# Optimization experiments

Hardware: AMD Instinct MI355X
Metric: run time of the kernel (lower is better)

## Reference

```python
import jax, jax.numpy as jnp
import numpy as np

FP4_MAX = 6.0
FP8_MAX = 448.0  # float8_e4m3fn max
BLOCK = 16
# representable |values| of fp4 e2m1 and decision midpoints (ties round up)
FP4_LEVELS = jnp.array([0.0, 0.5, 1.0, 1.5, 2.0, 3.0, 4.0, 6.0], dtype=jnp.float32)
FP4_MIDS = jnp.array([0.25, 0.75, 1.25, 1.75, 2.5, 3.5, 5.0], dtype=jnp.float32)


def _fp4_round(x):
    # round to nearest fp4 e2m1 value (magnitudes clamp at 6)
    a = jnp.abs(x)
    idx = jnp.searchsorted(FP4_MIDS, a, side='right')
    return jnp.sign(x) * FP4_LEVELS[idx]


def nvfp4_quant(x, global_scale):
    # x: [M, K] float32 -> (q_fp4 values [M, K], block scales [M, K//16] fp8-representable)
    M, K = x.shape
    xb = x.reshape(M, K // BLOCK, BLOCK)
    block_amax = jnp.max(jnp.abs(xb), axis=-1)  # [M, K//16]
    scale = jnp.clip(block_amax * (global_scale / FP4_MAX), 0.0, FP8_MAX)
    scale = scale.astype(jnp.float8_e4m3fn).astype(jnp.float32)
    safe = jnp.where(scale == 0.0, 1.0, scale)
    q = _fp4_round(xb * (global_scale / safe)[..., None])
    return q.reshape(M, K), scale


def setup_inputs() -> dict:
    key = jax.random.key(0)
    k_in, k_w, k_b = jax.random.split(key, 3)
    M, K, N = 256, 5120, 13824
    x = jax.random.normal(k_in, (M, K), dtype=jnp.float32)
    # build pre-quantized NVFP4 weight buffers (as the module's load_quantized_weights would)
    w = jax.random.normal(k_w, (N, K), dtype=jnp.float32) * 0.02
    w_gs = (FP8_MAX * FP4_MAX) / jnp.max(jnp.abs(w))  # scalar float32
    w_fp4, w_scale = nvfp4_quant(w, w_gs)
    bias = jax.random.normal(k_b, (N,), dtype=jnp.float32) * 0.01
    return {
        'input': x,
        'weight_fp4': w_fp4,            # [N, K] fp4 values held in f32
        'weight_scale': w_scale,        # [N, K//16] fp8_e4m3-representable f32
        'weight_global_scale': w_gs,    # scalar f32
        'bias': bias,                   # [N]
    }


def reference(input, weight_fp4, weight_scale, weight_global_scale, bias):
    # activations cast to bf16 (as in the torch module), math in f32
    x = input.astype(jnp.bfloat16).astype(jnp.float32)
    M, K = x.shape
    N = weight_fp4.shape[0]
    # per-tensor global scale for activations
    a_gs = (FP8_MAX * FP4_MAX) / jnp.max(jnp.abs(x))
    alpha = 1.0 / (a_gs * weight_global_scale)
    # on-the-fly fp4 quantization of activations
    a_fp4, a_scale = nvfp4_quant(x, a_gs)
    # block-scaled dequant-matmul: out = (a_fp4*s_a) @ (w_fp4*s_w)^T * alpha + bias
    a_u = (a_fp4.reshape(M, K // BLOCK, BLOCK) * a_scale[..., None]).reshape(M, K)
    w_u = (weight_fp4.reshape(N, K // BLOCK, BLOCK) * weight_scale[..., None]).reshape(N, K)
    out = jnp.einsum('mk,nk->mn', a_u, w_u) * alpha + bias[None, :]
    return out
```

## Files before the change

kernel.cpp:

```cpp
#include <hip/hip_runtime.h>

typedef __attribute__((ext_vector_type(8))) __bf16 bf16x8;
typedef __attribute__((ext_vector_type(4))) __bf16 bf16x4;
typedef __attribute__((ext_vector_type(4))) float floatx4;

#define M_TOT 256
#define K_TOT 5120
#define N_TOT 13824
#define NBLK  320
#define BN    64
#define BK    32
#define KSPLIT 4
#define KCH   1280
#define NSTEP 40

#define GLOAD_LDS16(g, l)                                                     \
  __builtin_amdgcn_global_load_lds(                                           \
      (const __attribute__((address_space(1))) void*)(g),                     \
      (__attribute__((address_space(3))) void*)(l), 16, 0, 0)

static __device__ __forceinline__ float bf16r(float v) { return (float)(__bf16)v; }

static __device__ __forceinline__ float fp4round(float v) {
  float a = fabsf(v), q;
  if      (a < 0.25f) q = 0.0f;
  else if (a < 0.75f) q = 0.5f;
  else if (a < 1.25f) q = 1.0f;
  else if (a < 1.75f) q = 1.5f;
  else if (a < 2.5f)  q = 2.0f;
  else if (a < 3.5f)  q = 3.0f;
  else if (a < 5.0f)  q = 4.0f;
  else                q = 6.0f;
  return copysignf(q, v);
}

static __device__ __forceinline__ float cvt_e4m3(float f) {
  if (f < 0.015625f) return rintf(f * 512.0f) * 0.001953125f;
  int e = (int)(__float_as_uint(f) >> 23) - 127;
  float q = __uint_as_float((unsigned)(e - 3 + 127) << 23);
  return rintf(f / q) * q;
}

__global__ void k_zero(float4* __restrict__ out4) {
  int idx = blockIdx.x * blockDim.x + threadIdx.x;
#pragma unroll
  for (int i = 0; i < 4; ++i) out4[idx + i * 221184] = (float4){0.f, 0.f, 0.f, 0.f};
}

__global__ void k_amax(const float* __restrict__ x, unsigned* __restrict__ amax_bits) {
  int i = blockIdx.x * blockDim.x + threadIdx.x;
  float4 v = ((const float4*)x)[i];
  float m = fmaxf(fmaxf(fabsf(bf16r(v.x)), fabsf(bf16r(v.y))),
                  fmaxf(fabsf(bf16r(v.z)), fabsf(bf16r(v.w))));
#pragma unroll
  for (int off = 32; off; off >>= 1) m = fmaxf(m, __shfl_xor(m, off));
  if ((threadIdx.x & 63) == 0) atomicMax(amax_bits, __float_as_uint(m));
}

__global__ void k_aquant(const float* __restrict__ x,
                         const unsigned* __restrict__ amax_bits,
                         __bf16* __restrict__ au) {
  int idx = blockIdx.x * blockDim.x + threadIdx.x;
  int m = idx / NBLK;
  int b = idx - m * NBLK;
  float amax = __uint_as_float(*amax_bits);
  float gs  = 2688.0f / amax;
  float gs6 = gs / 6.0f;
  const float4* xp = (const float4*)(x + m * K_TOT + b * 16);
  float4 v0 = xp[0], v1 = xp[1], v2 = xp[2], v3 = xp[3];
  float xv[16];
  xv[0]=bf16r(v0.x); xv[1]=bf16r(v0.y); xv[2]=bf16r(v0.z); xv[3]=bf16r(v0.w);
  xv[4]=bf16r(v1.x); xv[5]=bf16r(v1.y); xv[6]=bf16r(v1.z); xv[7]=bf16r(v1.w);
  xv[8]=bf16r(v2.x); xv[9]=bf16r(v2.y); xv[10]=bf16r(v2.z); xv[11]=bf16r(v2.w);
  xv[12]=bf16r(v3.x); xv[13]=bf16r(v3.y); xv[14]=bf16r(v3.z); xv[15]=bf16r(v3.w);
  float am = 0.f;
#pragma unroll
  for (int j = 0; j < 16; ++j) am = fmaxf(am, fabsf(xv[j]));
  float s = cvt_e4m3(fminf(am * gs6, 448.0f));
  float g = gs / ((s == 0.f) ? 1.f : s);
  bf16x8 p0, p1;
#pragma unroll
  for (int j = 0; j < 8; ++j) p0[j] = (__bf16)(fp4round(xv[j] * g) * s);
#pragma unroll
  for (int j = 0; j < 8; ++j) p1[j] = (__bf16)(fp4round(xv[8 + j] * g) * s);
  bf16x8* dst = (bf16x8*)(au + (size_t)idx * 16);
  dst[0] = p0; dst[1] = p1;
}

__global__ __launch_bounds__(512, 4) void k_gemm(
    const __bf16* __restrict__ au,
    const float*  __restrict__ w,
    const float*  __restrict__ wsc,
    const unsigned* __restrict__ amax_bits,
    const float*  __restrict__ wgs,
    const float*  __restrict__ bias,
    float* __restrict__ out)
{
  __shared__ __bf16 Ab[2][M_TOT * BK];
  __shared__ __bf16 Bb[2][BN * BK];

  const int tid  = threadIdx.x;
  const int lane = tid & 63;
  const int wv   = tid >> 6;
  const int wm   = wv >> 1;
  const int wn   = wv & 1;

  const int s     = blockIdx.x & (KSPLIT - 1);
  const int n0    = (blockIdx.x >> 2) * BN;
  const int kbase = s * KCH;

  const int arow  = wv * 32 + (lane >> 2);
  const int acolp = 8 * ((lane & 3) ^ ((lane >> 2) & 3));

  const int brow = tid >> 3;
  const int bcg  = tid & 7;
  const float* wp  = w   + (size_t)(n0 + brow) * K_TOT + kbase + bcg * 4;
  const float* wsp = wsc + (size_t)(n0 + brow) * NBLK + s * (KCH / 16);
  const int bsci = bcg >> 2;
  const int bdst = brow * 64 + (((bcg >> 1) ^ (brow & 3)) << 4) + (bcg & 1) * 8;

  const int hi  = lane >> 4;
  const int r15 = lane & 15;
  const int sw3 = r15 & 3;

  floatx4 acc[4][2];
#pragma unroll
  for (int fm = 0; fm < 4; ++fm)
#pragma unroll
    for (int fn = 0; fn < 2; ++fn) acc[fm][fn] = (floatx4){0.f, 0.f, 0.f, 0.f};

  float4 bv; float bs;

  auto issueA = [&](int t, int buf) {
    const __bf16* src = au + (size_t)arow * K_TOT + kbase + t * BK + acolp;
    char* dst = (char*)(&Ab[buf][0]) + wv * 2048;
#pragma unroll
    for (int i = 0; i < 2; ++i)
      GLOAD_LDS16(src + (size_t)i * 16 * K_TOT, dst + i * 1024);
  };
  auto loadB = [&](int t) {
    bv = *(const float4*)(wp + t * BK);
    bs = wsp[t * 2 + bsci];
  };
  auto writeB = [&](int buf) {
    bf16x4 pk;
    pk[0] = (__bf16)(bv.x * bs); pk[1] = (__bf16)(bv.y * bs);
    pk[2] = (__bf16)(bv.z * bs); pk[3] = (__bf16)(bv.w * bs);
    *(bf16x4*)((char*)(&Bb[buf][0]) + bdst) = pk;
  };
  auto compute = [&](int buf) {
    char* pA = (char*)(&Ab[buf][0]);
    char* pB = (char*)(&Bb[buf][0]);
    bf16x8 af[4], bfr[2];
#pragma unroll
    for (int fm = 0; fm < 4; ++fm) {
      const int row = wm * 64 + fm * 16 + r15;
      af[fm] = *(const bf16x8*)(pA + row * 64 + ((hi ^ sw3) << 4));
    }
#pragma unroll
    for (int fn = 0; fn < 2; ++fn) {
      const int row = wn * 32 + fn * 16 + r15;
      bfr[fn] = *(const bf16x8*)(pB + row * 64 + ((hi ^ sw3) << 4));
    }
#pragma unroll
    for (int fm = 0; fm < 4; ++fm)
#pragma unroll
      for (int fn = 0; fn < 2; ++fn)
        acc[fm][fn] = __builtin_amdgcn_mfma_f32_16x16x32_bf16(af[fm], bfr[fn], acc[fm][fn], 0, 0, 0);
  };

  int buf = 0;
  issueA(0, 0);
  loadB(0);
  writeB(0);
  __syncthreads();
#pragma unroll 1
  for (int t = 0; t < NSTEP; ++t) {
    if (t + 1 < NSTEP) { issueA(t + 1, buf ^ 1); loadB(t + 1); }
    compute(buf);
    if (t + 1 < NSTEP) writeB(buf ^ 1);
    __syncthreads();
    buf ^= 1;
  }

  float amax = __uint_as_float(*amax_bits);
  float a_gs = 2688.0f / amax;
  float alpha = 1.0f / (a_gs * wgs[0]);
#pragma unroll
  for (int fm = 0; fm < 4; ++fm) {
#pragma unroll
    for (int fn = 0; fn < 2; ++fn) {
      int mrow = wm * 64 + fm * 16 + hi * 4;
      int ncol = n0 + wn * 32 + fn * 16 + r15;
      float bb = (s == 0) ? bias[ncol] : 0.0f;
#pragma unroll
      for (int j = 0; j < 4; ++j)
        atomicAdd(&out[(size_t)(mrow + j) * N_TOT + ncol],
                  acc[fm][fn][j] * alpha + bb);
    }
  }
}

extern "C" void kernel_launch(void* const* d_in, const int* in_sizes, int n_in,
                              void* d_out, int out_size, void* d_ws, size_t ws_size,
                              hipStream_t stream) {
  const float* x    = (const float*)d_in[0];
  const float* wq   = (const float*)d_in[1];
  const float* wsc  = (const float*)d_in[2];
  const float* wgs  = (const float*)d_in[3];
  const float* bias = (const float*)d_in[4];
  float* out = (float*)d_out;

  unsigned* amax = (unsigned*)d_ws;
  __bf16* au = (__bf16*)((char*)d_ws + 256);

  hipMemsetAsync(d_ws, 0, 4, stream);
  k_zero<<<dim3(864), dim3(256), 0, stream>>>((float4*)out);
  k_amax<<<dim3(M_TOT * K_TOT / 4 / 256), dim3(256), 0, stream>>>(x, amax);
  k_aquant<<<dim3(M_TOT * NBLK / 256), dim3(256), 0, stream>>>(x, amax, au);
  k_gemm<<<dim3((N_TOT / BN) * KSPLIT), dim3(512), 0, stream>>>(au, wq, wsc, amax, wgs, bias, out);
}
```

Baseline: 245.9 us.

## Deepen GEMM pipeline to 4 LDS slots with manual waitcnt and fuse prep kernels

The GEMM main loop moves from a double-buffered scheme with __syncthreads to a 4-slot LDS ring that prefetches two K-steps ahead. It uses explicit s_waitcnt vmcnt/lgkmcnt and raw s_barrier with sched_barriers so global loads overlap compute across steps. The LDS swizzle changes to XOR on row>>1 bits to alter the bank-conflict pattern. The output-zeroing and amax kernels are fused into one launch to save launch overhead. LDS use doubles, which may reduce occupancy, and the hand-written waitcnt counts must match the number of outstanding loads.

```diff
diff --git a/kernel.cpp b/kernel.cpp
--- a/kernel.cpp
+++ b/kernel.cpp
@@ -41,15 +41,12 @@
   return rintf(f / q) * q;
 }
 
-__global__ void k_zero(float4* __restrict__ out4) {
+__global__ void k_prep(const float* __restrict__ x, unsigned* __restrict__ amax_bits,
+                       float4* __restrict__ out4) {
   int idx = blockIdx.x * blockDim.x + threadIdx.x;
-#pragma unroll
-  for (int i = 0; i < 4; ++i) out4[idx + i * 221184] = (float4){0.f, 0.f, 0.f, 0.f};
-}
-
-__global__ void k_amax(const float* __restrict__ x, unsigned* __restrict__ amax_bits) {
-  int i = blockIdx.x * blockDim.x + threadIdx.x;
-  float4 v = ((const float4*)x)[i];
+#pragma unroll 1
+  for (int j = idx; j < 884736; j += 327680) out4[j] = (float4){0.f, 0.f, 0.f, 0.f};
+  float4 v = ((const float4*)x)[idx];
   float m = fmaxf(fmaxf(fabsf(bf16r(v.x)), fabsf(bf16r(v.y))),
                   fmaxf(fabsf(bf16r(v.z)), fabsf(bf16r(v.w))));
 #pragma unroll
@@ -96,8 +93,8 @@
     const float*  __restrict__ bias,
     float* __restrict__ out)
 {
-  __shared__ __bf16 Ab[2][M_TOT * BK];
-  __shared__ __bf16 Bb[2][BN * BK];
+  __shared__ __bf16 Ab[4][M_TOT * BK];
+  __shared__ __bf16 Bb[4][BN * BK];
 
   const int tid  = threadIdx.x;
   const int lane = tid & 63;
@@ -110,18 +107,18 @@
   const int kbase = s * KCH;
 
   const int arow  = wv * 32 + (lane >> 2);
-  const int acolp = 8 * ((lane & 3) ^ ((lane >> 2) & 3));
+  const int acolp = 8 * ((lane & 3) ^ ((lane >> 3) & 3));
 
   const int brow = tid >> 3;
   const int bcg  = tid & 7;
   const float* wp  = w   + (size_t)(n0 + brow) * K_TOT + kbase + bcg * 4;
   const float* wsp = wsc + (size_t)(n0 + brow) * NBLK + s * (KCH / 16);
   const int bsci = bcg >> 2;
-  const int bdst = brow * 64 + (((bcg >> 1) ^ (brow & 3)) << 4) + (bcg & 1) * 8;
+  const int bdst = brow * 64 + (((bcg >> 1) ^ ((brow >> 1) & 3)) << 4) + (bcg & 1) * 8;
 
   const int hi  = lane >> 4;
   const int r15 = lane & 15;
-  const int sw3 = r15 & 3;
+  const int rsw = (r15 >> 1) & 3;
 
   floatx4 acc[4][2];
 #pragma unroll
@@ -129,38 +126,31 @@
 #pragma unroll
     for (int fn = 0; fn < 2; ++fn) acc[fm][fn] = (floatx4){0.f, 0.f, 0.f, 0.f};
 
-  float4 bv; float bs;
-
-  auto issueA = [&](int t, int buf) {
+  auto issueA = [&](int t, int slot) {
     const __bf16* src = au + (size_t)arow * K_TOT + kbase + t * BK + acolp;
-    char* dst = (char*)(&Ab[buf][0]) + wv * 2048;
-#pragma unroll
-    for (int i = 0; i < 2; ++i)
-      GLOAD_LDS16(src + (size_t)i * 16 * K_TOT, dst + i * 1024);
+    char* dst = (char*)(&Ab[slot][0]) + wv * 2048;
+    GLOAD_LDS16(src, dst);
+    GLOAD_LDS16(src + (size_t)16 * K_TOT, dst + 1024);
   };
-  auto loadB = [&](int t) {
-    bv = *(const float4*)(wp + t * BK);
-    bs = wsp[t * 2 + bsci];
-  };
-  auto writeB = [&](int buf) {
+  auto writeB = [&](float4 bv, float bs, int slot) {
     bf16x4 pk;
     pk[0] = (__bf16)(bv.x * bs); pk[1] = (__bf16)(bv.y * bs);
     pk[2] = (__bf16)(bv.z * bs); pk[3] = (__bf16)(bv.w * bs);
-    *(bf16x4*)((char*)(&Bb[buf][0]) + bdst) = pk;
+    *(bf16x4*)((char*)(&Bb[slot][0]) + bdst) = pk;
   };
-  auto compute = [&](int buf) {
-    char* pA = (char*)(&Ab[buf][0]);
-    char* pB = (char*)(&Bb[buf][0]);
+  auto compute = [&](int slot) {
+    char* pA = (char*)(&Ab[slot][0]);
+    char* pB = (char*)(&Bb[slot][0]);
     bf16x8 af[4], bfr[2];
 #pragma unroll
     for (int fm = 0; fm < 4; ++fm) {
       const int row = wm * 64 + fm * 16 + r15;
-      af[fm] = *(const bf16x8*)(pA + row * 64 + ((hi ^ sw3) << 4));
+      af[fm] = *(const bf16x8*)(pA + row * 64 + ((hi ^ rsw) << 4));
     }
 #pragma unroll
     for (int fn = 0; fn < 2; ++fn) {
       const int row = wn * 32 + fn * 16 + r15;
-      bfr[fn] = *(const bf16x8*)(pB + row * 64 + ((hi ^ sw3) << 4));
+      bfr[fn] = *(const bf16x8*)(pB + row * 64 + ((hi ^ rsw) << 4));
     }
 #pragma unroll
     for (int fm = 0; fm < 4; ++fm)
@@ -169,18 +159,47 @@
         acc[fm][fn] = __builtin_amdgcn_mfma_f32_16x16x32_bf16(af[fm], bfr[fn], acc[fm][fn], 0, 0, 0);
   };
 
-  int buf = 0;
+  float4 bvA, bvB; float bsA, bsB;
+
   issueA(0, 0);
-  loadB(0);
-  writeB(0);
-  __syncthreads();
+  bvA = *(const float4*)(wp);          bsA = wsp[bsci];
+  issueA(1, 1);
+  bvB = *(const float4*)(wp + BK);     bsB = wsp[2 + bsci];
+  asm volatile("s_waitcnt vmcnt(4)" ::: "memory");
+  writeB(bvA, bsA, 0);
+
 #pragma unroll 1
-  for (int t = 0; t < NSTEP; ++t) {
-    if (t + 1 < NSTEP) { issueA(t + 1, buf ^ 1); loadB(t + 1); }
-    compute(buf);
-    if (t + 1 < NSTEP) writeB(buf ^ 1);
-    __syncthreads();
-    buf ^= 1;
+  for (int t = 0; t < NSTEP; t += 2) {
+    if (t + 2 < NSTEP) {
+      issueA(t + 2, (t + 2) & 3);
+      bvA = *(const float4*)(wp + (t + 2) * BK);
+      bsA = wsp[(t + 2) * 2 + bsci];
+      asm volatile("s_waitcnt vmcnt(4)" ::: "memory");
+    } else {
+      asm volatile("s_waitcnt vmcnt(0)" ::: "memory");
+    }
+    writeB(bvB, bsB, (t + 1) & 3);
+    asm volatile("s_waitcnt lgkmcnt(0)" ::: "memory");
+    __builtin_amdgcn_sched_barrier(0);
+    __builtin_amdgcn_s_barrier();
+    __builtin_amdgcn_sched_barrier(0);
+    compute(t & 3);
+
+    if (t + 3 < NSTEP) {
+      issueA(t + 3, (t + 3) & 3);
+      bvB = *(const float4*)(wp + (t + 3) * BK);
+      bsB = wsp[(t + 3) * 2 + bsci];
+      asm volatile("s_waitcnt vmcnt(4)" ::: "memory");
+      writeB(bvA, bsA, (t + 2) & 3);
+    } else if (t + 2 < NSTEP) {
+      asm volatile("s_waitcnt vmcnt(0)" ::: "memory");
+      writeB(bvA, bsA, (t + 2) & 3);
+    }
+    asm volatile("s_waitcnt lgkmcnt(0)" ::: "memory");
+    __builtin_amdgcn_sched_barrier(0);
+    __builtin_amdgcn_s_barrier();
+    __builtin_amdgcn_sched_barrier(0);
+    compute((t + 1) & 3);
   }
 
   float amax = __uint_as_float(*amax_bits);
@@ -215,8 +234,7 @@
   __bf16* au = (__bf16*)((char*)d_ws + 256);
 
   hipMemsetAsync(d_ws, 0, 4, stream);
-  k_zero<<<dim3(864), dim3(256), 0, stream>>>((float4*)out);
-  k_amax<<<dim3(M_TOT * K_TOT / 4 / 256), dim3(256), 0, stream>>>(x, amax);
+  k_prep<<<dim3(1280), dim3(256), 0, stream>>>(x, amax, (float4*)out);
   k_aquant<<<dim3(M_TOT * NBLK / 256), dim3(256), 0, stream>>>(x, amax, au);
   k_gemm<<<dim3((N_TOT / BN) * KSPLIT), dim3(512), 0, stream>>>(au, wq, wsc, amax, wgs, bias, out);
 }
```

After: 237.3 us. -3.5%, faster.
